# Optimization experiments

Measured on AMD Instinct MI355X. Metric: run time of the kernel, lower is better.

## Reference

```python
import jax, jax.numpy as jnp
import numpy as np

KERNEL = 9
STRIDE = 2
NUM_ITERS = 3


def squash(s):
    # Matches the module: norm over last dim; v = ||s|| / (1 + ||s||^2) * s
    n = jnp.linalg.norm(s, axis=-1, keepdims=True)
    return n / (1.0 + n * n) * s


def setup_inputs() -> dict:
    key = jax.random.key(0)
    k1, k2, k3 = jax.random.split(key, 3)
    B, nc, ic, oc, H = 32, 32, 256, 32, 71  # H'=(71-9)//2+1 = 32 = B = nc = oc (required by the original broadcasting)
    x = jax.random.normal(k1, (B, ic, H, H), dtype=jnp.float32)
    # Conv2d default init: U(-1/sqrt(fan_in), 1/sqrt(fan_in)), fan_in = ic*9*9
    bound = 1.0 / np.sqrt(ic * KERNEL * KERNEL)
    W = jax.random.uniform(k2, (nc, oc, ic, KERNEL, KERNEL), jnp.float32, -bound, bound)
    b = jax.random.uniform(k3, (nc, oc), jnp.float32, -bound, bound)
    return {"x": x, "W": W, "b": b}


def reference(x, W, b):
    nc, oc, ic = W.shape[0], W.shape[1], W.shape[2]
    # All nc per-capsule convs fused into one grouped output-channel conv
    Wf = W.reshape(nc * oc, ic, KERNEL, KERNEL)
    u = jax.lax.conv_general_dilated(
        x, Wf, window_strides=(STRIDE, STRIDE), padding='VALID',
        dimension_numbers=('NCHW', 'OIHW', 'NCHW'))
    B = u.shape[0]
    Hp, Wp = u.shape[2], u.shape[3]
    u_hat = u.reshape(B, nc, oc, Hp, Wp) + b[None, :, :, None, None]  # [B,nc,oc,Hp,Wp]

    # Dynamic routing. The torch code initializes b_ij as rank-4 zeros; because
    # softmax(0) is uniform and 0 + agreement == agreement, this rank-5 zero init
    # is numerically identical and shape-clean.
    b_ij = jnp.zeros((B, nc, oc, Hp, 1), dtype=u_hat.dtype)
    v = None
    for it in range(NUM_ITERS):
        c = jax.nn.softmax(b_ij, axis=1)                  # over capsule dim
        s = (c * u_hat).sum(axis=2, keepdims=True)        # [B,nc,1,Hp,Wp]
        v = squash(s)
        if it < NUM_ITERS - 1:
            b_ij = b_ij + (u_hat * v).sum(axis=-1, keepdims=True)  # [B,nc,oc,Hp,1]
    # torch returns v_j.squeeze(-1): last dim is Wp != 1 so it is a no-op
    return v  # [B, nc, 1, Hp, Wp]
```

## Files before the change

### kernel.cpp

```cpp
#include <hip/hip_runtime.h>
#include <cstdint>
#include <cstddef>

typedef unsigned short u16;
typedef signed char s8;
typedef __attribute__((ext_vector_type(4))) int i32x4;

#define XT_HSTRIDE 18432
#define XT_BSTRIDE 1308672
#define K_TOT 20736
#define N_TOT 32768
#define NKT 324
#define S_X (5.0f / 127.0f)

__device__ __forceinline__ u16 f2bf(float f) {
  uint32_t u = __builtin_bit_cast(uint32_t, f);
  u = (u + 0x7fffu + ((u >> 16) & 1u)) >> 16;
  return (u16)u;
}
__device__ __forceinline__ float bf2f(u16 h) {
  uint32_t u = ((uint32_t)h) << 16;
  return __builtin_bit_cast(float, u);
}

__device__ __forceinline__ void gl_lds16(const s8* g, s8* l) {
  __builtin_amdgcn_global_load_lds((const __attribute__((address_space(1))) void*)g,
                                   (__attribute__((address_space(3))) void*)l, 16, 0, 0);
}

__device__ __forceinline__ void wg_barrier() {
  asm volatile("" ::: "memory");
  __builtin_amdgcn_s_barrier();
  asm volatile("" ::: "memory");
}

__device__ __forceinline__ void koffs(int kt, int& ka, int& kb) {
  const int pos = kt >> 2;
  const int cq = kt & 3;
  const int kh = pos / 9;
  const int kw = pos - kh * 9;
  ka = kt * 64;
  kb = kh * XT_HSTRIDE + (kw & 1) * 9216 + (kw >> 1) * 256 + cq * 64;
}

__global__ __launch_bounds__(256) void pack_w(const float* __restrict__ W,
                                              s8* __restrict__ Wb,
                                              float* __restrict__ sw) {
  __shared__ __align__(16) s8 wl[20736];
  __shared__ float red[256];
  const int m = blockIdx.x;
  const int t = threadIdx.x;
  const size_t base = (size_t)m * K_TOT;
  const float4* W4 = (const float4*)(W + base);
  float mx = 0.f;
  for (int i = t; i < 5184; i += 256) {
    float4 v = W4[i];
    mx = fmaxf(mx, fmaxf(fmaxf(fabsf(v.x), fabsf(v.y)),
                         fmaxf(fabsf(v.z), fabsf(v.w))));
  }
  red[t] = mx;
  __syncthreads();
  for (int s = 128; s > 0; s >>= 1) {
    if (t < s) red[t] = fmaxf(red[t], red[t + s]);
    __syncthreads();
  }
  const float amax = fmaxf(red[0], 1e-20f);
  const float inv = 127.0f / amax;
  if (t == 0) sw[m] = amax * (1.0f / 127.0f);
  for (int i = t; i < K_TOT; i += 256) {
    float f = W[base + i];
    int c = i / 81;
    int pos = i - c * 81;
    wl[pos * 256 + c] = (s8)__float2int_rn(f * inv);
  }
  __syncthreads();
  const uint4* s4 = (const uint4*)wl;
  uint4* d4 = (uint4*)(Wb + base);
  for (int i = t; i < 1296; i += 256) d4[i] = s4[i];
}

__global__ __launch_bounds__(256) void pack_x(const float* __restrict__ X,
                                              s8* __restrict__ xT) {
  __shared__ s8 xl[71 * 260];
  const int h = blockIdx.x;
  const int b = blockIdx.y;
  const int t = threadIdx.x;
  for (int i = t; i < 256 * 71; i += 256) {
    int c = i / 71;
    int w = i - c * 71;
    float f = X[(((size_t)(b * 256 + c)) * 71 + h) * 71 + w];
    f = fminf(fmaxf(f, -5.f), 5.f) * 25.4f;
    xl[w * 260 + c] = (s8)__float2int_rn(f);
  }
  __syncthreads();
  const size_t obase = (size_t)b * XT_BSTRIDE + (size_t)h * XT_HSTRIDE;
  const int c4 = t & 63;
  const int g = t >> 6;
  for (int s = g; s < 71; s += 4) {
    int par = (s >= 36) ? 1 : 0;
    int j = s - par * 36;
    int w = 2 * j + par;
    uint32_t d = *(const uint32_t*)&xl[w * 260 + 4 * c4];
    *(uint32_t*)&xT[obase + par * 9216 + j * 256 + 4 * c4] = d;
  }
}

__global__ __launch_bounds__(512, 2) void conv_gemm(const s8* __restrict__ Wb,
                                                    const s8* __restrict__ xT,
                                                    const float* __restrict__ sw,
                                                    u16* __restrict__ U) {
  __shared__ __align__(16) s8 As[2][2][256 * 64];
  __shared__ __align__(16) s8 Bs[2][2][256 * 64];
  const int tid = threadIdx.x;
  const int bx = blockIdx.x;
  const int swz = (bx & 7) * 64 + (bx >> 3);
  const int m0 = (swz & 3) * 256;
  const int n0 = (swz >> 2) * 256;
  const int lane = tid & 63;
  const int wave = tid >> 6;
  const int wm = wave >> 2;
  const int wn = wave & 3;

  const int rl2 = lane >> 2;
  const int gch16 = ((lane & 3) ^ ((rl2 >> 1) & 3)) * 16;

  const s8* aS[2];
  const s8* bS[2];
#pragma unroll
  for (int j = 0; j < 2; ++j) {
    const int row = j * 128 + wave * 16 + rl2;
    aS[j] = Wb + (size_t)(m0 + row) * K_TOT + gch16;
    const int n = n0 + row;
    const size_t nb = (size_t)(n >> 10) * XT_BSTRIDE +
                      (size_t)(((n >> 5) & 31) * 2) * XT_HSTRIDE +
                      (size_t)(n & 31) * 256;
    bS[j] = xT + nb + gch16;
  }
  const int sdst = wave * 16 * 64 + lane * 16;

  i32x4 acc[8][4];
#pragma unroll
  for (int i = 0; i < 8; ++i)
#pragma unroll
    for (int j = 0; j < 4; ++j) acc[i][j] = (i32x4){0, 0, 0, 0};

  const int fr = lane & 15;
  const int q4 = lane >> 4;
  const int cph = ((q4 ^ ((fr >> 1) & 3))) * 16;
  int offA[8], offB[4];
#pragma unroll
  for (int mi = 0; mi < 8; ++mi)
    offA[mi] = (wm * 128 + (mi & 3) * 16 + (mi >> 2) * 64 + fr) * 64 + cph;
#pragma unroll
  for (int j = 0; j < 4; ++j)
    offB[j] = (wn * 64 + j * 16 + fr) * 64 + cph;

  {
    int ka0, kb0, ka1, kb1;
    koffs(0, ka0, kb0);
    koffs(1, ka1, kb1);
    gl_lds16(bS[0] + kb0, &Bs[0][0][0 * 8192 + sdst]);
    gl_lds16(bS[1] + kb0, &Bs[0][0][1 * 8192 + sdst]);
    gl_lds16(bS[0] + kb1, &Bs[0][1][0 * 8192 + sdst]);
    gl_lds16(bS[1] + kb1, &Bs[0][1][1 * 8192 + sdst]);
    gl_lds16(aS[0] + ka0, &As[0][0][0 * 8192 + sdst]);
    gl_lds16(aS[1] + ka0, &As[0][0][1 * 8192 + sdst]);
    gl_lds16(aS[0] + ka1, &As[0][1][0 * 8192 + sdst]);
    gl_lds16(aS[1] + ka1, &As[0][1][1 * 8192 + sdst]);
  }

#pragma unroll 1
  for (int it2 = 0; it2 < NKT / 2; ++it2) {
    const int sp = it2 & 1;
    const bool more = (it2 + 1 < NKT / 2);
    int ka0n = 0, kb0n = 0, ka1n = 0, kb1n = 0;
    if (more) {
      koffs(2 * it2 + 2, ka0n, kb0n);
      koffs(2 * it2 + 3, ka1n, kb1n);
    }
    const s8* Ac0 = &As[sp][0][0];
    const s8* Bc0 = &Bs[sp][0][0];
    const s8* Ac1 = &As[sp][1][0];
    const s8* Bc1 = &Bs[sp][1][0];
    s8* An0 = &As[sp ^ 1][0][0];
    s8* Bn0 = &Bs[sp ^ 1][0][0];
    s8* An1 = &As[sp ^ 1][1][0];
    s8* Bn1 = &Bs[sp ^ 1][1][0];

    asm volatile("s_waitcnt vmcnt(0)" ::: "memory");
    wg_barrier();

    i32x4 aF[8], bF[4];

#pragma unroll
    for (int j = 0; j < 4; ++j) bF[j] = *(const i32x4*)(Bc0 + offB[j]);
#pragma unroll
    for (int mi = 0; mi < 4; ++mi) aF[mi] = *(const i32x4*)(Ac0 + offA[mi]);
    if (more) {
      gl_lds16(bS[0] + kb0n, Bn0 + 0 * 8192 + sdst);
      gl_lds16(bS[1] + kb0n, Bn0 + 1 * 8192 + sdst);
    }
    __builtin_amdgcn_sched_barrier(0);
    __builtin_amdgcn_s_setprio(1);
#pragma unroll
    for (int mi = 0; mi < 4; ++mi)
#pragma unroll
      for (int j = 0; j < 4; ++j)
        acc[mi][j] = __builtin_amdgcn_mfma_i32_16x16x64_i8(aF[mi], bF[j], acc[mi][j], 0, 0, 0);
    __builtin_amdgcn_s_setprio(0);
    __builtin_amdgcn_sched_barrier(0);

#pragma unroll
    for (int mi = 4; mi < 8; ++mi) aF[mi] = *(const i32x4*)(Ac0 + offA[mi]);
    if (more) {
      gl_lds16(bS[0] + kb1n, Bn1 + 0 * 8192 + sdst);
      gl_lds16(bS[1] + kb1n, Bn1 + 1 * 8192 + sdst);
    }
    __builtin_amdgcn_sched_barrier(0);
    __builtin_amdgcn_s_setprio(1);
#pragma unroll
    for (int mi = 4; mi < 8; ++mi)
#pragma unroll
      for (int j = 0; j < 4; ++j)
        acc[mi][j] = __builtin_amdgcn_mfma_i32_16x16x64_i8(aF[mi], bF[j], acc[mi][j], 0, 0, 0);
    __builtin_amdgcn_s_setprio(0);
    __builtin_amdgcn_sched_barrier(0);

#pragma unroll
    for (int j = 0; j < 4; ++j) bF[j] = *(const i32x4*)(Bc1 + offB[j]);
#pragma unroll
    for (int mi = 0; mi < 4; ++mi) aF[mi] = *(const i32x4*)(Ac1 + offA[mi]);
    if (more) {
      gl_lds16(aS[0] + ka0n, An0 + 0 * 8192 + sdst);
      gl_lds16(aS[1] + ka0n, An0 + 1 * 8192 + sdst);
    }
    __builtin_amdgcn_sched_barrier(0);
    __builtin_amdgcn_s_setprio(1);
#pragma unroll
    for (int mi = 0; mi < 4; ++mi)
#pragma unroll
      for (int j = 0; j < 4; ++j)
        acc[mi][j] = __builtin_amdgcn_mfma_i32_16x16x64_i8(aF[mi], bF[j], acc[mi][j], 0, 0, 0);
    __builtin_amdgcn_s_setprio(0);
    __builtin_amdgcn_sched_barrier(0);

#pragma unroll
    for (int mi = 4; mi < 8; ++mi) aF[mi] = *(const i32x4*)(Ac1 + offA[mi]);
    if (more) {
      gl_lds16(aS[0] + ka1n, An1 + 0 * 8192 + sdst);
      gl_lds16(aS[1] + ka1n, An1 + 1 * 8192 + sdst);
    }
    __builtin_amdgcn_sched_barrier(0);
    __builtin_amdgcn_s_setprio(1);
#pragma unroll
    for (int mi = 4; mi < 8; ++mi)
#pragma unroll
      for (int j = 0; j < 4; ++j)
        acc[mi][j] = __builtin_amdgcn_mfma_i32_16x16x64_i8(aF[mi], bF[j], acc[mi][j], 0, 0, 0);
    __builtin_amdgcn_s_setprio(0);
  }

  const int r0 = (lane >> 4) * 4;
  const int cn = lane & 15;
#pragma unroll
  for (int mi = 0; mi < 8; ++mi) {
    const int mgb = m0 + wm * 128 + (mi & 3) * 16 + (mi >> 2) * 64 + r0;
    float ds[4];
#pragma unroll
    for (int r = 0; r < 4; ++r) ds[r] = sw[mgb + r] * S_X;
#pragma unroll
    for (int j = 0; j < 4; ++j) {
      const int ng = n0 + wn * 64 + j * 16 + cn;
#pragma unroll
      for (int r = 0; r < 4; ++r)
        U[(size_t)(mgb + r) * N_TOT + ng] = f2bf((float)acc[mi][j][r] * ds[r]);
    }
  }
}

__global__ __launch_bounds__(1024) void routing_k(const u16* __restrict__ U,
                                                  const float* __restrict__ bias,
                                                  float* __restrict__ out) {
  const int t = threadIdx.x;
  const int bx = blockIdx.x;
  const int b = bx >> 5;
  const int hp = bx & 31;
  const int oc = t & 31;
  const int nc = t >> 5;
  __shared__ float sm[1024];

  float u_r[32];
  {
    const uint4* up4 = (const uint4*)(U + (size_t)t * N_TOT + b * 1024 + hp * 32);
    const float bs = bias[t];
#pragma unroll
    for (int i = 0; i < 4; ++i) {
      uint4 q = up4[i];
      uint32_t vv[4] = {q.x, q.y, q.z, q.w};
#pragma unroll
      for (int k = 0; k < 4; ++k) {
        u_r[i * 8 + k * 2]     = bf2f((u16)(vv[k] & 0xffffu)) + bs;
        u_r[i * 8 + k * 2 + 1] = bf2f((u16)(vv[k] >> 16)) + bs;
      }
    }
  }

  float bij = 0.f;
  float s[32];
  float scale = 0.f;

  for (int it = 0; it < 3; ++it) {
    sm[t] = bij;
    __syncthreads();
    float den = 0.f;
#pragma unroll
    for (int i = 0; i < 32; ++i) den += __expf(sm[i * 32 + oc]);
    const float c = __expf(bij) / den;
#pragma unroll
    for (int w = 0; w < 32; ++w) s[w] = c * u_r[w];
#pragma unroll
    for (int off = 1; off < 32; off <<= 1) {
#pragma unroll
      for (int w = 0; w < 32; ++w) s[w] += __shfl_xor(s[w], off, 64);
    }
    float n2 = 0.f;
#pragma unroll
    for (int w = 0; w < 32; ++w) n2 += s[w] * s[w];
    scale = sqrtf(n2) / (1.f + n2);
    if (it < 2) {
      float agr = 0.f;
#pragma unroll
      for (int w = 0; w < 32; ++w) agr += u_r[w] * s[w];
      bij += scale * agr;
    }
    __syncthreads();
  }

  float val = s[0];
#pragma unroll
  for (int i = 1; i < 32; ++i) val = (oc == i) ? s[i] : val;
  out[(size_t)((b * 32 + nc) * 32 + hp) * 32 + oc] = scale * val;
}

extern "C" void kernel_launch(void* const* d_in, const int* in_sizes, int n_in,
                              void* d_out, int out_size, void* d_ws, size_t ws_size,
                              hipStream_t stream) {
  const float* x = (const float*)d_in[0];
  const float* W = (const float*)d_in[1];
  const float* bias = (const float*)d_in[2];

  s8*    Wb = (s8*)d_ws;
  float* sw = (float*)((char*)d_ws + 21233664u);
  s8*    xT = (s8*)((char*)d_ws + 21237760u);
  u16*   U  = (u16*)((char*)d_ws + 63115264u);
  float* out = (float*)d_out;

  pack_w<<<dim3(1024), dim3(256), 0, stream>>>(W, Wb, sw);
  pack_x<<<dim3(71, 32), dim3(256), 0, stream>>>(x, xT);
  conv_gemm<<<dim3(512), dim3(512), 0, stream>>>(Wb, xT, sw, U);
  routing_k<<<dim3(1024), dim3(1024), 0, stream>>>(U, bias, out);
}
```

Measured before the change: 997.0 us.

## Rework weight packing, drop GEMM sched barriers, specialize first routing iteration

The weight-pack kernel now keeps each thread's 81 weights in registers after the max pass instead of re-reading global memory. It writes to a padded LDS layout (stride 264) to reduce bank conflicts and stores with uint2 copies. The GEMM main loop drops the sched_barrier after each async LDS prefetch, giving the compiler freedom to interleave those loads with the MFMAs. The routing kernel special-cases the first iteration with uniform coefficients, computes exp once per thread rather than 32 times per reader, and skips a trailing barrier. The padded stores and the register array may raise LDS or register pressure, and freer scheduling could reorder MFMA issue unfavourably.

```diff
diff --git a/kernel.cpp b/kernel.cpp
--- a/kernel.cpp
+++ b/kernel.cpp
@@ -46,17 +46,17 @@
 __global__ __launch_bounds__(256) void pack_w(const float* __restrict__ W,
                                               s8* __restrict__ Wb,
                                               float* __restrict__ sw) {
-  __shared__ __align__(16) s8 wl[20736];
+  __shared__ __align__(16) s8 wl[81 * 264];
   __shared__ float red[256];
   const int m = blockIdx.x;
   const int t = threadIdx.x;
   const size_t base = (size_t)m * K_TOT;
-  const float4* W4 = (const float4*)(W + base);
+  float r[81];
   float mx = 0.f;
-  for (int i = t; i < 5184; i += 256) {
-    float4 v = W4[i];
-    mx = fmaxf(mx, fmaxf(fmaxf(fabsf(v.x), fabsf(v.y)),
-                         fmaxf(fabsf(v.z), fabsf(v.w))));
+#pragma unroll
+  for (int k = 0; k < 81; ++k) {
+    r[k] = W[base + t + k * 256];
+    mx = fmaxf(mx, fabsf(r[k]));
   }
   red[t] = mx;
   __syncthreads();
@@ -67,16 +67,20 @@
   const float amax = fmaxf(red[0], 1e-20f);
   const float inv = 127.0f / amax;
   if (t == 0) sw[m] = amax * (1.0f / 127.0f);
-  for (int i = t; i < K_TOT; i += 256) {
-    float f = W[base + i];
-    int c = i / 81;
-    int pos = i - c * 81;
-    wl[pos * 256 + c] = (s8)__float2int_rn(f * inv);
+#pragma unroll
+  for (int k = 0; k < 81; ++k) {
+    const int i = t + k * 256;
+    const int c = i / 81;
+    const int pos = i - c * 81;
+    wl[pos * 264 + c] = (s8)__float2int_rn(r[k] * inv);
   }
   __syncthreads();
-  const uint4* s4 = (const uint4*)wl;
-  uint4* d4 = (uint4*)(Wb + base);
-  for (int i = t; i < 1296; i += 256) d4[i] = s4[i];
+  for (int idx = t; idx < 81 * 32; idx += 256) {
+    const int pos = idx >> 5;
+    const int cq = idx & 31;
+    *(uint2*)(Wb + base + pos * 256 + cq * 8) =
+        *(const uint2*)(wl + pos * 264 + cq * 8);
+  }
 }
 
 __global__ __launch_bounds__(256) void pack_x(const float* __restrict__ X,
@@ -200,7 +204,6 @@
       gl_lds16(bS[0] + kb0n, Bn0 + 0 * 8192 + sdst);
       gl_lds16(bS[1] + kb0n, Bn0 + 1 * 8192 + sdst);
     }
-    __builtin_amdgcn_sched_barrier(0);
     __builtin_amdgcn_s_setprio(1);
 #pragma unroll
     for (int mi = 0; mi < 4; ++mi)
@@ -216,7 +219,6 @@
       gl_lds16(bS[0] + kb1n, Bn1 + 0 * 8192 + sdst);
       gl_lds16(bS[1] + kb1n, Bn1 + 1 * 8192 + sdst);
     }
-    __builtin_amdgcn_sched_barrier(0);
     __builtin_amdgcn_s_setprio(1);
 #pragma unroll
     for (int mi = 4; mi < 8; ++mi)
@@ -234,7 +236,6 @@
       gl_lds16(aS[0] + ka0n, An0 + 0 * 8192 + sdst);
       gl_lds16(aS[1] + ka0n, An0 + 1 * 8192 + sdst);
     }
-    __builtin_amdgcn_sched_barrier(0);
     __builtin_amdgcn_s_setprio(1);
 #pragma unroll
     for (int mi = 0; mi < 4; ++mi)
@@ -250,7 +251,6 @@
       gl_lds16(aS[0] + ka1n, An1 + 0 * 8192 + sdst);
       gl_lds16(aS[1] + ka1n, An1 + 1 * 8192 + sdst);
     }
-    __builtin_amdgcn_sched_barrier(0);
     __builtin_amdgcn_s_setprio(1);
 #pragma unroll
     for (int mi = 4; mi < 8; ++mi)
@@ -286,7 +286,6 @@
   const int b = bx >> 5;
   const int hp = bx & 31;
   const int oc = t & 31;
-  const int nc = t >> 5;
   __shared__ float sm[1024];
 
   float u_r[32];
@@ -309,13 +308,32 @@
   float s[32];
   float scale = 0.f;
 
-  for (int it = 0; it < 3; ++it) {
-    sm[t] = bij;
+  {
+    const float c = 1.0f / 32.0f;
+#pragma unroll
+    for (int w = 0; w < 32; ++w) s[w] = c * u_r[w];
+#pragma unroll
+    for (int off = 1; off < 32; off <<= 1) {
+#pragma unroll
+      for (int w = 0; w < 32; ++w) s[w] += __shfl_xor(s[w], off, 64);
+    }
+    float n2 = 0.f;
+#pragma unroll
+    for (int w = 0; w < 32; ++w) n2 += s[w] * s[w];
+    scale = sqrtf(n2) / (1.f + n2);
+    float agr = 0.f;
+#pragma unroll
+    for (int w = 0; w < 32; ++w) agr += u_r[w] * s[w];
+    bij += scale * agr;
+  }
+
+  for (int it = 1; it < 3; ++it) {
+    sm[t] = __expf(bij);
     __syncthreads();
     float den = 0.f;
 #pragma unroll
-    for (int i = 0; i < 32; ++i) den += __expf(sm[i * 32 + oc]);
-    const float c = __expf(bij) / den;
+    for (int i = 0; i < 32; ++i) den += sm[i * 32 + oc];
+    const float c = sm[t] / den;
 #pragma unroll
     for (int w = 0; w < 32; ++w) s[w] = c * u_r[w];
 #pragma unroll
@@ -332,10 +350,11 @@
 #pragma unroll
       for (int w = 0; w < 32; ++w) agr += u_r[w] * s[w];
       bij += scale * agr;
-    }
-    __syncthreads();
-  }
-
+      __syncthreads();
+    }
+  }
+
+  const int nc = t >> 5;
   float val = s[0];
 #pragma unroll
   for (int i = 1; i < 32; ++i) val = (oc == i) ? s[i] : val;
```

Measured after the change: 939.8 us. 5.7% less time.
